# Optimization experiments

Hardware: AMD Instinct MI355X
Metric: run time of the kernel (lower is better)

The kernel has to match this reference:

```python
import jax, jax.numpy as jnp
import numpy as np

TEMPERATURE = 8.0  # sqrt(d_k=64)

def setup_inputs() -> dict:
    key = jax.random.key(0)
    kq, kk, kv = jax.random.split(key, 3)
    B, S, D = 32, 2048, 64
    q = jax.random.normal(kq, (B, S, D), dtype=jnp.float32)
    k = jax.random.normal(kk, (B, S, D), dtype=jnp.float32)
    v = jax.random.normal(kv, (B, S, D), dtype=jnp.float32)
    return {"q": q, "k": k, "v": v}

def reference(q, k, v):
    # scores: [B, S_q, S_k]
    attn = jnp.einsum('bqd,bkd->bqk', q, k) / TEMPERATURE
    attn = jax.nn.softmax(attn, axis=2)
    # dropout is identity in eval mode (deterministic reference baseline)
    output = jnp.einsum('bqk,bkd->bqd', attn, v)
    return (output, attn)
```

## Files before the change

### kernel.cpp

```cpp
#include <hip/hip_runtime.h>
#include <cstdint>
#include <cstddef>

#define B_    32
#define S_    2048
#define D_    64
#define QBLK  16
#define SP    2056

typedef __attribute__((ext_vector_type(8))) short short8_t;
typedef __attribute__((ext_vector_type(4))) float f32x4;

__device__ __forceinline__ short f2bf(float f) {
  union { float f; unsigned u; } x; x.f = f;
  unsigned u = x.u;
  u += 0x7fffu + ((u >> 16) & 1u);
  return (short)(u >> 16);
}
__device__ __forceinline__ float bf2f(unsigned s) {
  union { unsigned u; float f; } x;
  x.u = (s & 0xffffu) << 16;
  return x.f;
}

__global__ void convert_bf16_kernel(const float* __restrict__ in,
                                    short* __restrict__ out, int n4) {
  int i = blockIdx.x * blockDim.x + threadIdx.x;
  if (i >= n4) return;
  f32x4 f = ((const f32x4*)in)[i];
  short4 o;
  o.x = f2bf(f[0]); o.y = f2bf(f[1]); o.z = f2bf(f[2]); o.w = f2bf(f[3]);
  ((short4*)out)[i] = o;
}

__global__ void transpose_v_kernel(const float* __restrict__ v,
                                   short* __restrict__ vt) {
  __shared__ float t[64][65];
  int b   = blockIdx.x >> 5;
  int st  = blockIdx.x & 31;
  int tid = threadIdx.x;
  const float* src = v + ((size_t)(b * S_ + st * 64)) * D_;
#pragma unroll
  for (int p = 0; p < 4; ++p) {
    int r = p * 16 + (tid >> 4);
    int c = (tid & 15) * 4;
    f32x4 f = *(const f32x4*)(src + (size_t)r * D_ + c);
    t[r][c] = f[0]; t[r][c+1] = f[1]; t[r][c+2] = f[2]; t[r][c+3] = f[3];
  }
  __syncthreads();
#pragma unroll
  for (int p = 0; p < 8; ++p) {
    int d  = p * 8 + (tid >> 5);
    int si = (tid & 31) * 2;
    unsigned lo = (unsigned short)f2bf(t[si][d]);
    unsigned hi = (unsigned short)f2bf(t[si + 1][d]);
    *(unsigned*)(vt + ((size_t)(b * D_ + d)) * S_ + st * 64 + si) = lo | (hi << 16);
  }
}

template <bool WS>
__global__ __launch_bounds__(512, 4)
void attn_kernel(const float* __restrict__ q, const float* __restrict__ k,
                 const float* __restrict__ v, const short* __restrict__ Kb,
                 const short* __restrict__ Vt, float* __restrict__ out,
                 float* __restrict__ attn) {
  __shared__ short P_lds[QBLK][SP];
  __shared__ float redmax[QBLK][8];
  __shared__ float redsum[QBLK][8];
  __shared__ float Ored[4][16][17];

  const int tid  = threadIdx.x;
  const int lane = tid & 63;
  const int wv   = tid >> 6;
  const int lr   = lane & 15;
  const int lq   = lane >> 4;

  const int nwg  = gridDim.x;
  const int per  = nwg >> 3;
  const int bid0 = blockIdx.x;
  const int bid  = (bid0 & 7) * per + (bid0 >> 3);

  const int b     = bid >> 7;
  const int qbase = (bid & 127) * QBLK;

  short8_t qf[2];
  {
    const float* qp = q + ((size_t)(b * S_ + qbase + lr)) * D_ + lq * 8;
#pragma unroll
    for (int kp = 0; kp < 2; ++kp) {
      f32x4 f0 = *(const f32x4*)(qp + kp * 32);
      f32x4 f1 = *(const f32x4*)(qp + kp * 32 + 4);
      short8_t a;
      a[0] = f2bf(f0[0]); a[1] = f2bf(f0[1]); a[2] = f2bf(f0[2]); a[3] = f2bf(f0[3]);
      a[4] = f2bf(f1[0]); a[5] = f2bf(f1[1]); a[6] = f2bf(f1[2]); a[7] = f2bf(f1[3]);
      qf[kp] = a;
    }
  }

  f32x4 acc[16];
#pragma unroll
  for (int ct = 0; ct < 16; ++ct) acc[ct] = (f32x4){0.f, 0.f, 0.f, 0.f};

  const int wcol = wv * 256;
#pragma unroll
  for (int ct = 0; ct < 16; ++ct) {
    int n = wcol + ct * 16 + lr;
    short8_t b0, b1;
    if constexpr (WS) {
      const short* kr = Kb + ((size_t)(b * S_ + n)) * D_ + lq * 8;
      b0 = *(const short8_t*)(kr);
      b1 = *(const short8_t*)(kr + 32);
    } else {
      const float* kr = k + ((size_t)(b * S_ + n)) * D_ + lq * 8;
      f32x4 f0 = *(const f32x4*)(kr);
      f32x4 f1 = *(const f32x4*)(kr + 4);
      f32x4 f2 = *(const f32x4*)(kr + 32);
      f32x4 f3 = *(const f32x4*)(kr + 36);
      b0[0]=f2bf(f0[0]); b0[1]=f2bf(f0[1]); b0[2]=f2bf(f0[2]); b0[3]=f2bf(f0[3]);
      b0[4]=f2bf(f1[0]); b0[5]=f2bf(f1[1]); b0[6]=f2bf(f1[2]); b0[7]=f2bf(f1[3]);
      b1[0]=f2bf(f2[0]); b1[1]=f2bf(f2[1]); b1[2]=f2bf(f2[2]); b1[3]=f2bf(f2[3]);
      b1[4]=f2bf(f3[0]); b1[5]=f2bf(f3[1]); b1[6]=f2bf(f3[2]); b1[7]=f2bf(f3[3]);
    }
    acc[ct] = __builtin_amdgcn_mfma_f32_16x16x32_bf16(b0, qf[0], acc[ct], 0, 0, 0);
    acc[ct] = __builtin_amdgcn_mfma_f32_16x16x32_bf16(b1, qf[1], acc[ct], 0, 0, 0);
  }

  float m = acc[0][0];
#pragma unroll
  for (int ct = 0; ct < 16; ++ct)
#pragma unroll
    for (int i = 0; i < 4; ++i) m = fmaxf(m, acc[ct][i]);
  m = fmaxf(m, __shfl_xor(m, 16));
  m = fmaxf(m, __shfl_xor(m, 32));
  if (lane < 16) redmax[lr][wv] = m;
  __syncthreads();
  float mf = redmax[lr][0];
#pragma unroll
  for (int w2 = 1; w2 < 8; ++w2) mf = fmaxf(mf, redmax[lr][w2]);

  float s = 0.f;
#pragma unroll
  for (int ct = 0; ct < 16; ++ct)
#pragma unroll
    for (int i = 0; i < 4; ++i) {
      float p = __expf((acc[ct][i] - mf) * 0.125f);
      acc[ct][i] = p;
      s += p;
    }
  s += __shfl_xor(s, 16);
  s += __shfl_xor(s, 32);
  if (lane < 16) redsum[lr][wv] = s;
  __syncthreads();
  float sum = 0.f;
#pragma unroll
  for (int w2 = 0; w2 < 8; ++w2) sum += redsum[lr][w2];
  const float rl = 1.f / sum;

#pragma unroll
  for (int ct = 0; ct < 16; ++ct) {
    unsigned lo = (unsigned)(unsigned short)f2bf(acc[ct][0] * rl) |
                  ((unsigned)(unsigned short)f2bf(acc[ct][1] * rl) << 16);
    unsigned hi = (unsigned)(unsigned short)f2bf(acc[ct][2] * rl) |
                  ((unsigned)(unsigned short)f2bf(acc[ct][3] * rl) << 16);
    uint2 pk; pk.x = lo; pk.y = hi;
    *(uint2*)&P_lds[lr][wcol + ct * 16 + lq * 4] = pk;
  }
  __syncthreads();

  const int cc = wv & 3;
  const int hh = wv >> 2;
  const int dbase = cc * 16;
  f32x4 oacc = (f32x4){0.f, 0.f, 0.f, 0.f};
  const short* vrow = WS ? (Vt + ((size_t)(b * D_ + dbase + lr)) * S_ + hh * 1024)
                         : nullptr;
#pragma unroll 4
  for (int st2 = 0; st2 < 32; ++st2) {
    int kidx = st2 * 32 + lq * 8;
    short8_t p0 = *(const short8_t*)&P_lds[lr][hh * 1024 + kidx];
    short8_t vb;
    if constexpr (WS) {
      vb = *(const short8_t*)(vrow + kidx);
    } else {
#pragma unroll
      for (int e = 0; e < 8; ++e)
        vb[e] = f2bf(v[((size_t)(b * S_ + hh * 1024 + kidx + e)) * D_ + dbase + lr]);
    }
    oacc = __builtin_amdgcn_mfma_f32_16x16x32_bf16(p0, vb, oacc, 0, 0, 0);
  }
  if (hh == 1) {
#pragma unroll
    for (int i = 0; i < 4; ++i)
      Ored[cc][lq * 4 + i][lr] = oacc[i];
  }
  __syncthreads();
  if (hh == 0) {
#pragma unroll
    for (int i = 0; i < 4; ++i) {
      float o = oacc[i] + Ored[cc][lq * 4 + i][lr];
      out[((size_t)(b * S_ + qbase + lq * 4 + i)) * D_ + dbase + lr] = o;
    }
  }

  {
    const int r0 = wv * 2;
#pragma unroll
    for (int rr = 0; rr < 2; ++rr) {
      const int r = r0 + rr;
      float* arow = attn + ((size_t)b * S_ + qbase + r) * S_;
#pragma unroll
      for (int it = 0; it < 8; ++it) {
        const int col = it * 256 + lane * 4;
        uint2 pk = *(const uint2*)&P_lds[r][col];
        f32x4 o;
        o[0] = bf2f(pk.x);
        o[1] = bf2f(pk.x >> 16);
        o[2] = bf2f(pk.y);
        o[3] = bf2f(pk.y >> 16);
        __builtin_nontemporal_store(o, (f32x4*)(arow + col));
      }
    }
  }
}

extern "C" void kernel_launch(void* const* d_in, const int* in_sizes, int n_in,
                              void* d_out, int out_size, void* d_ws, size_t ws_size,
                              hipStream_t stream) {
  (void)in_sizes; (void)n_in; (void)out_size;
  const float* q = (const float*)d_in[0];
  const float* k = (const float*)d_in[1];
  const float* v = (const float*)d_in[2];
  float* out  = (float*)d_out;
  float* attn = out + (size_t)B_ * S_ * D_;

  const size_t nelem = (size_t)B_ * S_ * D_;
  const size_t need  = nelem * 2 * sizeof(short);

  dim3 grid(B_ * (S_ / QBLK));
  if (d_ws != nullptr && ws_size >= need) {
    short* Kb = (short*)d_ws;
    short* Vt = Kb + nelem;
    convert_bf16_kernel<<<(int)((nelem / 4 + 255) / 256), 256, 0, stream>>>(k, Kb, (int)(nelem / 4));
    transpose_v_kernel<<<B_ * (S_ / 64), 256, 0, stream>>>(v, Vt);
    attn_kernel<true><<<grid, 512, 0, stream>>>(q, k, v, Kb, Vt, out, attn);
  } else {
    attn_kernel<false><<<grid, 512, 0, stream>>>(q, k, v, nullptr, nullptr, out, attn);
  }
}
```

Before: 285.3 us.

## Split attention probability write into bf16 workspace plus separate expand kernel

When the workspace is large enough, the attention kernel writes normalized probabilities as bf16 into a workspace buffer instead of expanding them to fp32 in place. A separate grid-stride kernel then reads the bf16 buffer and writes the fp32 attention matrix with nontemporal stores. The aim is to shorten the main kernel's store tail and let a simple streaming kernel saturate write bandwidth. The cost is an extra 256MB round trip through memory and an extra launch, and it only takes effect if the harness supplies a large enough workspace.

```diff
diff --git a/kernel.cpp b/kernel.cpp
--- a/kernel.cpp
+++ b/kernel.cpp
@@ -10,6 +10,8 @@
 
 typedef __attribute__((ext_vector_type(8))) short short8_t;
 typedef __attribute__((ext_vector_type(4))) float f32x4;
+typedef __attribute__((ext_vector_type(2))) unsigned u32x2;
+typedef __attribute__((ext_vector_type(4))) unsigned u32x4;
 
 __device__ __forceinline__ short f2bf(float f) {
   union { float f; unsigned u; } x; x.f = f;
@@ -58,12 +60,28 @@
   }
 }
 
-template <bool WS>
+__global__ __launch_bounds__(256)
+void expand_kernel(const unsigned* __restrict__ P, float* __restrict__ attn,
+                   long n4) {
+  long i      = (long)blockIdx.x * blockDim.x + threadIdx.x;
+  long stride = (long)gridDim.x * blockDim.x;
+  for (; i < n4; i += stride) {
+    u32x2 pk = __builtin_nontemporal_load((const u32x2*)P + i);
+    f32x4 o;
+    o[0] = bf2f(pk[0]);
+    o[1] = bf2f(pk[0] >> 16);
+    o[2] = bf2f(pk[1]);
+    o[3] = bf2f(pk[1] >> 16);
+    __builtin_nontemporal_store(o, (f32x4*)attn + i);
+  }
+}
+
+template <bool WS, bool SPLIT>
 __global__ __launch_bounds__(512, 4)
 void attn_kernel(const float* __restrict__ q, const float* __restrict__ k,
                  const float* __restrict__ v, const short* __restrict__ Kb,
                  const short* __restrict__ Vt, float* __restrict__ out,
-                 float* __restrict__ attn) {
+                 float* __restrict__ attn, short* __restrict__ Pws) {
   __shared__ short P_lds[QBLK][SP];
   __shared__ float redmax[QBLK][8];
   __shared__ float redsum[QBLK][8];
@@ -162,8 +180,8 @@
                   ((unsigned)(unsigned short)f2bf(acc[ct][1] * rl) << 16);
     unsigned hi = (unsigned)(unsigned short)f2bf(acc[ct][2] * rl) |
                   ((unsigned)(unsigned short)f2bf(acc[ct][3] * rl) << 16);
-    uint2 pk; pk.x = lo; pk.y = hi;
-    *(uint2*)&P_lds[lr][wcol + ct * 16 + lq * 4] = pk;
+    u32x2 pk; pk[0] = lo; pk[1] = hi;
+    *(u32x2*)&P_lds[lr][wcol + ct * 16 + lq * 4] = pk;
   }
   __syncthreads();
 
@@ -206,17 +224,27 @@
 #pragma unroll
     for (int rr = 0; rr < 2; ++rr) {
       const int r = r0 + rr;
-      float* arow = attn + ((size_t)b * S_ + qbase + r) * S_;
-#pragma unroll
-      for (int it = 0; it < 8; ++it) {
-        const int col = it * 256 + lane * 4;
-        uint2 pk = *(const uint2*)&P_lds[r][col];
-        f32x4 o;
-        o[0] = bf2f(pk.x);
-        o[1] = bf2f(pk.x >> 16);
-        o[2] = bf2f(pk.y);
-        o[3] = bf2f(pk.y >> 16);
-        __builtin_nontemporal_store(o, (f32x4*)(arow + col));
+      if constexpr (SPLIT) {
+        short* prow = Pws + ((size_t)(b * S_ + qbase + r)) * S_;
+#pragma unroll
+        for (int it = 0; it < 4; ++it) {
+          const int col = it * 512 + lane * 8;
+          u32x4 pk = *(const u32x4*)&P_lds[r][col];
+          __builtin_nontemporal_store(pk, (u32x4*)(prow + col));
+        }
+      } else {
+        float* arow = attn + ((size_t)b * S_ + qbase + r) * S_;
+#pragma unroll
+        for (int it = 0; it < 8; ++it) {
+          const int col = it * 256 + lane * 4;
+          u32x2 pk = *(const u32x2*)&P_lds[r][col];
+          f32x4 o;
+          o[0] = bf2f(pk[0]);
+          o[1] = bf2f(pk[0] >> 16);
+          o[2] = bf2f(pk[1]);
+          o[3] = bf2f(pk[1] >> 16);
+          __builtin_nontemporal_store(o, (f32x4*)(arow + col));
+        }
       }
     }
   }
@@ -232,17 +260,27 @@
   float* out  = (float*)d_out;
   float* attn = out + (size_t)B_ * S_ * D_;
 
-  const size_t nelem = (size_t)B_ * S_ * D_;
-  const size_t need  = nelem * 2 * sizeof(short);
+  const size_t nelem  = (size_t)B_ * S_ * D_;
+  const size_t needKV = nelem * 2 * sizeof(short);
+  const size_t nP     = (size_t)B_ * S_ * S_;
+  const size_t needP  = nP * sizeof(short);
 
   dim3 grid(B_ * (S_ / QBLK));
-  if (d_ws != nullptr && ws_size >= need) {
+  if (d_ws != nullptr && ws_size >= needKV + needP) {
+    short* Kb  = (short*)d_ws;
+    short* Vt  = Kb + nelem;
+    short* Pws = Vt + nelem;
+    convert_bf16_kernel<<<(int)((nelem / 4 + 255) / 256), 256, 0, stream>>>(k, Kb, (int)(nelem / 4));
+    transpose_v_kernel<<<B_ * (S_ / 64), 256, 0, stream>>>(v, Vt);
+    attn_kernel<true, true><<<grid, 512, 0, stream>>>(q, k, v, Kb, Vt, out, attn, Pws);
+    expand_kernel<<<2048, 256, 0, stream>>>((const unsigned*)Pws, attn, (long)(nP / 4));
+  } else if (d_ws != nullptr && ws_size >= needKV) {
     short* Kb = (short*)d_ws;
     short* Vt = Kb + nelem;
     convert_bf16_kernel<<<(int)((nelem / 4 + 255) / 256), 256, 0, stream>>>(k, Kb, (int)(nelem / 4));
     transpose_v_kernel<<<B_ * (S_ / 64), 256, 0, stream>>>(v, Vt);
-    attn_kernel<true><<<grid, 512, 0, stream>>>(q, k, v, Kb, Vt, out, attn);
+    attn_kernel<true, false><<<grid, 512, 0, stream>>>(q, k, v, Kb, Vt, out, attn, nullptr);
   } else {
-    attn_kernel<false><<<grid, 512, 0, stream>>>(q, k, v, nullptr, nullptr, out, attn);
-  }
-}
+    attn_kernel<false, false><<<grid, 512, 0, stream>>>(q, k, v, nullptr, nullptr, out, attn, nullptr);
+  }
+}
```

New measurement: 417.9 us. +46.5%, slower.
